# Performance work log

Hardware: AMD Instinct MI355X
Metric: run time of the kernel (lower is better)

The kernel has to match this reference:

```python
import jax, jax.numpy as jnp
import numpy as np

EPS_BN = 1e-5
EPS_W = 1e-8


def _bn(x, g, b, m, v):
    # x: [B, N, C]; params: [C] (inference-mode batchnorm)
    return g * (x - m) * jax.lax.rsqrt(v + EPS_BN) + b


def setup_inputs() -> dict:
    key = jax.random.key(0)
    ks = jax.random.split(key, 24)
    B, N, S = 16, 4096, 1024
    C1, C2 = 128, 256            # points1 / points2 channels
    CIN, COUT = C1 + C2, 128     # in_channel, out_channel

    def w(k, shape, std=0.02):
        return (jax.random.normal(k, shape, jnp.float32) * std)

    def bn_params(k, c):
        k1, k2, k3, k4 = jax.random.split(k, 4)
        return (1.0 + 0.1 * jax.random.normal(k1, (c,), jnp.float32),  # gamma
                0.1 * jax.random.normal(k2, (c,), jnp.float32),        # beta
                0.1 * jax.random.normal(k3, (c,), jnp.float32),        # running mean
                0.5 + jax.random.uniform(k4, (c,), jnp.float32))       # running var

    fg, fb, fm, fv = bn_params(ks[4], COUT)
    g1, b1, m1, v1 = bn_params(ks[5], COUT)
    g2, b2, m2, v2 = bn_params(ks[6], COUT)
    return {
        "xyz1": jax.random.uniform(ks[0], (B, N, 3), jnp.float32),
        "xyz2": jax.random.uniform(ks[1], (B, S, 3), jnp.float32),
        "points1": jax.random.normal(ks[2], (B, C1, N), jnp.float32),
        "points2": jax.random.normal(ks[3], (B, C2, S), jnp.float32),
        "fuse_w": w(ks[7], (COUT, CIN)), "fuse_b": jnp.zeros((COUT,), jnp.float32),
        "fuse_g": fg, "fuse_beta": fb, "fuse_m": fm, "fuse_v": fv,
        "c1_w": w(ks[8], (COUT, COUT)), "c1_b": jnp.zeros((COUT,), jnp.float32),
        "bn1_g": g1, "bn1_b": b1, "bn1_m": m1, "bn1_v": v1,
        "c2_w": w(ks[9], (COUT, COUT)), "c2_b": jnp.zeros((COUT,), jnp.float32),
        "bn2_g": g2, "bn2_b": b2, "bn2_m": m2, "bn2_v": v2,
    }


def reference(xyz1, xyz2, points1, points2,
              fuse_w, fuse_b, fuse_g, fuse_beta, fuse_m, fuse_v,
              c1_w, c1_b, bn1_g, bn1_b, bn1_m, bn1_v,
              c2_w, c2_b, bn2_g, bn2_b, bn2_m, bn2_v):
    B, N, _ = xyz1.shape
    pts1 = jnp.swapaxes(points1, 1, 2)   # [B, N, C1]
    pts2 = jnp.swapaxes(points2, 1, 2)   # [B, S, C2]

    # squared pairwise distances [B, N, S]
    dists = (jnp.sum(xyz1 ** 2, -1)[:, :, None]
             + jnp.sum(xyz2 ** 2, -1)[:, None, :]
             - 2.0 * jnp.einsum('bnc,bsc->bns', xyz1, xyz2))

    # 3 nearest neighbors (smallest distances)
    neg_d3, idx = jax.lax.top_k(-dists, 3)          # [B, N, 3]
    d3 = -neg_d3
    recip = 1.0 / (d3 + EPS_W)
    weight = recip / jnp.sum(recip, axis=2, keepdims=True)  # [B, N, 3]

    gathered = jax.vmap(lambda p, i: p[i])(pts2, idx)        # [B, N, 3, C2]
    interp = jnp.sum(gathered * weight[..., None], axis=2)   # [B, N, C2]

    x = jnp.concatenate([pts1, interp], axis=-1)             # [B, N, CIN]

    # fuse: 1x1 conv + BN + ReLU
    x = jax.nn.relu(_bn(jnp.einsum('bnc,oc->bno', x, fuse_w) + fuse_b,
                        fuse_g, fuse_beta, fuse_m, fuse_v))

    # residual block: conv-BN-ReLU -> conv-BN, add skip, ReLU
    h = jax.nn.relu(_bn(jnp.einsum('bnc,oc->bno', x, c1_w) + c1_b,
                        bn1_g, bn1_b, bn1_m, bn1_v))
    y = _bn(jnp.einsum('bnc,oc->bno', h, c2_w) + c2_b,
            bn2_g, bn2_b, bn2_m, bn2_v)
    out = jax.nn.relu(y + x)                                 # [B, N, COUT]
    return jnp.swapaxes(out, 1, 2)                           # [B, COUT, N]
```

## Files before the change

kernel.cpp:

```cpp
#include <hip/hip_runtime.h>
#include <hip/hip_bf16.h>

#define BB 16
#define NN 4096
#define SS 1024
#define C1 128
#define C2 256
#define CIN 384
#define CO 128

#define KCH 4
#define SCH (SS / KCH)

typedef __bf16 bf16x8 __attribute__((ext_vector_type(8)));
typedef float f32x4 __attribute__((ext_vector_type(4)));

__global__ __launch_bounds__(256) void knn_part_kernel(
    const float* __restrict__ xyz1, const float* __restrict__ xyz2,
    float4* __restrict__ pd4, int4* __restrict__ pi4)
{
    __shared__ float4 pts[SCH];
    const int b = blockIdx.z;
    const int ch = blockIdx.y;
    const float* p2 = xyz2 + ((size_t)b * SS + (size_t)ch * SCH) * 3;
    for (int i = threadIdx.x; i < SCH; i += 256) {
        float x = p2[i * 3 + 0], y = p2[i * 3 + 1], z = p2[i * 3 + 2];
        pts[i] = make_float4(x, y, z, x * x + y * y + z * z);
    }
    __syncthreads();

    const int n = blockIdx.x * 256 + threadIdx.x;
    const float* p1 = xyz1 + ((size_t)b * NN + n) * 3;
    const float x = p1[0], y = p1[1], z = p1[2];
    const float s1 = x * x + y * y + z * z;

    float d0 = 3.4e38f, d1 = 3.4e38f, d2 = 3.4e38f, d3 = 3.4e38f;
    int i0 = 0, i1 = 0, i2 = 0, i3 = 0;
    const int sbase = ch * SCH;
    #pragma unroll 4
    for (int sl = 0; sl < SCH; ++sl) {
        float4 p = pts[sl];
        float d = s1 + p.w - 2.0f * (x * p.x + y * p.y + z * p.z);
        int s = sbase + sl;
        bool lt0 = d < d0, lt1 = d < d1, lt2 = d < d2, lt3 = d < d3;
        float nd3 = lt2 ? d2 : (lt3 ? d : d3); int ni3 = lt2 ? i2 : (lt3 ? s : i3);
        float nd2 = lt1 ? d1 : (lt2 ? d : d2); int ni2 = lt1 ? i1 : (lt2 ? s : i2);
        float nd1 = lt0 ? d0 : (lt1 ? d : d1); int ni1 = lt0 ? i0 : (lt1 ? s : i1);
        d0 = lt0 ? d : d0;                     i0 = lt0 ? s : i0;
        d1 = nd1; i1 = ni1; d2 = nd2; i2 = ni2; d3 = nd3; i3 = ni3;
    }
    size_t o = ((size_t)b * NN + n) * KCH + ch;
    pd4[o] = make_float4(d0, d1, d2, d3);
    pi4[o] = make_int4(i0, i1, i2, i3);
}

__global__ __launch_bounds__(256) void knn_merge_kernel(
    const float4* __restrict__ pd4, const int4* __restrict__ pi4,
    int* __restrict__ idx4, float* __restrict__ w4)
{
    const int n = blockIdx.x * 256 + threadIdx.x;
    const int b = blockIdx.y;
    const size_t o = ((size_t)b * NN + n) * KCH;

    float d0 = 3.4e38f, d1 = 3.4e38f, d2 = 3.4e38f, d3 = 3.4e38f;
    int i0 = 0, i1 = 0, i2 = 0, i3 = 0;
    #pragma unroll
    for (int ch = 0; ch < KCH; ++ch) {
        float4 pd = pd4[o + ch];
        int4 pi = pi4[o + ch];
        float cd[4] = { pd.x, pd.y, pd.z, pd.w };
        int   ci[4] = { pi.x, pi.y, pi.z, pi.w };
        #pragma unroll
        for (int k = 0; k < 4; ++k) {
            float d = cd[k]; int s = ci[k];
            bool lt0 = d < d0, lt1 = d < d1, lt2 = d < d2, lt3 = d < d3;
            float nd3 = lt2 ? d2 : (lt3 ? d : d3); int ni3 = lt2 ? i2 : (lt3 ? s : i3);
            float nd2 = lt1 ? d1 : (lt2 ? d : d2); int ni2 = lt1 ? i1 : (lt2 ? s : i2);
            float nd1 = lt0 ? d0 : (lt1 ? d : d1); int ni1 = lt0 ? i0 : (lt1 ? s : i1);
            d0 = lt0 ? d : d0;                     i0 = lt0 ? s : i0;
            d1 = nd1; i1 = ni1; d2 = nd2; i2 = ni2; d3 = nd3; i3 = ni3;
        }
    }
    float r0 = 1.0f / (d0 + 1e-8f);
    float r1 = 1.0f / (d1 + 1e-8f);
    float r2 = 1.0f / (d2 + 1e-8f);
    float rs = r0 + r1 + r2;
    bool tie = (d2 == d3);
    size_t base = ((size_t)b * NN + n) * 4;
    idx4[base + 0] = i0; idx4[base + 1] = i1;
    idx4[base + 2] = i2; idx4[base + 3] = i3;
    w4[base + 0] = r0 / rs; w4[base + 1] = r1 / rs;
    w4[base + 2] = r2 / rs; w4[base + 3] = tie ? -1.0f : 0.0f;
}

__global__ __launch_bounds__(256) void p2t_kernel(
    const float* __restrict__ p2, float* __restrict__ p2t)
{
    __shared__ float tile[64][65];
    const int b = blockIdx.z;
    const int s0 = blockIdx.x * 64, c0 = blockIdx.y * 64;
    for (int i = threadIdx.x; i < 64 * 64; i += 256) {
        int s = i & 63, c = i >> 6;
        tile[c][s] = p2[((size_t)b * C2 + c0 + c) * SS + s0 + s];
    }
    __syncthreads();
    for (int i = threadIdx.x; i < 64 * 64; i += 256) {
        int c = i & 63, s = i >> 6;
        p2t[((size_t)b * SS + s0 + s) * C2 + c0 + c] = tile[c][s];
    }
}

__global__ __launch_bounds__(256) void wprep_kernel(
    const float* __restrict__ fw, const float* __restrict__ w1,
    const float* __restrict__ w2,
    __bf16* __restrict__ Whf, __bf16* __restrict__ Wlf,
    __bf16* __restrict__ Wh1, __bf16* __restrict__ Wl1,
    __bf16* __restrict__ Wh2, __bf16* __restrict__ Wl2)
{
    int t = blockIdx.x * 256 + threadIdx.x;
    float v; __bf16 *oh, *ol; int idx;
    if (t < 49152)      { idx = t;         v = fw[idx]; oh = Whf; ol = Wlf; }
    else if (t < 65536) { idx = t - 49152; v = w1[idx]; oh = Wh1; ol = Wl1; }
    else                { idx = t - 65536; v = w2[idx]; oh = Wh2; ol = Wl2; }
    __bf16 h = (__bf16)v;
    oh[idx] = h; ol[idx] = (__bf16)(v - (float)h);
}

__global__ __launch_bounds__(256) void tie_eval_kernel(
    const float* __restrict__ p2t, const float* __restrict__ points1,
    const int* __restrict__ idx4, float* __restrict__ w4,
    const float* __restrict__ fw, const float* __restrict__ fb,
    const float* __restrict__ fg, const float* __restrict__ fbt,
    const float* __restrict__ fm, const float* __restrict__ fv,
    const float* __restrict__ w1m, const float* __restrict__ b1,
    const float* __restrict__ g1, const float* __restrict__ bt1,
    const float* __restrict__ m1, const float* __restrict__ v1,
    const float* __restrict__ w2m, const float* __restrict__ b2,
    const float* __restrict__ g2, const float* __restrict__ bt2,
    const float* __restrict__ m2, const float* __restrict__ v2)
{
    __shared__ float Xs[4][2][CIN];
    __shared__ float XT[4][2][CO];
    __shared__ float Hs[4][2][CO];
    const int wave = threadIdx.x >> 6, lane = threadIdx.x & 63;
    const int n = blockIdx.x * 4 + wave;
    const int b = blockIdx.y;
    const size_t base = ((size_t)b * NN + n) * 4;
    if (w4[base + 3] != -1.0f) return;

    const int i0 = idx4[base + 0], i1 = idx4[base + 1];
    const int i2 = idx4[base + 2], i3 = idx4[base + 3];
    const float w0 = w4[base + 0], w1 = w4[base + 1], w2 = w4[base + 2];
    const float* P = p2t + (size_t)b * SS * C2;

    for (int c = lane; c < C1; c += 64) {
        float v = points1[((size_t)b * C1 + c) * NN + n];
        Xs[wave][0][c] = v; Xs[wave][1][c] = v;
    }
    for (int c = lane; c < C2; c += 64) {
        float f0 = P[(size_t)i0 * C2 + c], f1 = P[(size_t)i1 * C2 + c];
        float f2 = P[(size_t)i2 * C2 + c], f3 = P[(size_t)i3 * C2 + c];
        float bs = w0 * f0 + w1 * f1;
        Xs[wave][0][C1 + c] = bs + w2 * f2;
        Xs[wave][1][C1 + c] = bs + w2 * f3;
    }
    #pragma unroll
    for (int k = 0; k < 2; ++k) {
        int oc = lane + 64 * k;
        float alo = fb[oc], ahi = fb[oc];
        for (int c = 0; c < CIN; ++c) {
            float wv = fw[(size_t)oc * CIN + c];
            alo += wv * Xs[wave][0][c];
            ahi += wv * Xs[wave][1][c];
        }
        float s = fg[oc] * (1.0f / sqrtf(fv[oc] + 1e-5f));
        XT[wave][0][oc] = fmaxf(s * (alo - fm[oc]) + fbt[oc], 0.0f);
        XT[wave][1][oc] = fmaxf(s * (ahi - fm[oc]) + fbt[oc], 0.0f);
    }
    #pragma unroll
    for (int k = 0; k < 2; ++k) {
        int oc = lane + 64 * k;
        float alo = b1[oc], ahi = b1[oc];
        for (int c = 0; c < CO; ++c) {
            float wv = w1m[(size_t)oc * CO + c];
            alo += wv * XT[wave][0][c];
            ahi += wv * XT[wave][1][c];
        }
        float s = g1[oc] * (1.0f / sqrtf(v1[oc] + 1e-5f));
        Hs[wave][0][oc] = fmaxf(s * (alo - m1[oc]) + bt1[oc], 0.0f);
        Hs[wave][1][oc] = fmaxf(s * (ahi - m1[oc]) + bt1[oc], 0.0f);
    }
    float e = 0.0f;
    #pragma unroll
    for (int k = 0; k < 2; ++k) {
        int oc = lane + 64 * k;
        float alo = b2[oc], ahi = b2[oc];
        for (int c = 0; c < CO; ++c) {
            float wv = w2m[(size_t)oc * CO + c];
            alo += wv * Hs[wave][0][c];
            ahi += wv * Hs[wave][1][c];
        }
        float s = g2[oc] * (1.0f / sqrtf(v2[oc] + 1e-5f));
        float olo = fmaxf(s * (alo - m2[oc]) + bt2[oc] + XT[wave][0][oc], 0.0f);
        float ohi = fmaxf(s * (ahi - m2[oc]) + bt2[oc] + XT[wave][1][oc], 0.0f);
        e = fmaxf(e, fabsf(olo - ohi));
    }
    for (int off = 32; off; off >>= 1) e = fmaxf(e, __shfl_xor(e, off));
    if (lane == 0) {
        if (e > 0.085f) { w4[base + 3] = 0.0f; }
        else { w4[base + 2] = 0.5f * w2; w4[base + 3] = 0.5f * w2; }
    }
}

__global__ __launch_bounds__(256) void buildx_kernel(
    const float* __restrict__ points1,
    const float* __restrict__ p2t,
    const int* __restrict__ idx4, const float* __restrict__ w4,
    __bf16* __restrict__ Xh, __bf16* __restrict__ Xl)
{
    __shared__ float t1[128][66];
    const int b = blockIdx.y;
    const int n0 = blockIdx.x * 64;
    for (int i = threadIdx.x; i < 128 * 64; i += 256) {
        int j = i & 63, c = i >> 6;
        t1[c][j] = points1[((size_t)b * C1 + c) * NN + n0 + j];
    }
    __syncthreads();
    for (int i = threadIdx.x; i < 128 * 64; i += 256) {
        int c = i & 127, j = i >> 7;
        float v = t1[c][j];
        __bf16 h = (__bf16)v;
        size_t o = ((size_t)b * NN + n0 + j) * CIN + c;
        Xh[o] = h; Xl[o] = (__bf16)(v - (float)h);
    }
    for (int i = threadIdx.x; i < 64 * C2; i += 256) {
        int c = i & 255, j = i >> 8;
        int n = n0 + j;
        size_t ib = ((size_t)b * NN + n) * 4;
        int s0 = idx4[ib + 0], s1 = idx4[ib + 1];
        int s2 = idx4[ib + 2], s3 = idx4[ib + 3];
        float w0 = w4[ib + 0], w1 = w4[ib + 1];
        float w2 = w4[ib + 2], w3 = w4[ib + 3];
        const float* base = p2t + (size_t)b * SS * C2;
        float v = w0 * base[(size_t)s0 * C2 + c]
                + w1 * base[(size_t)s1 * C2 + c]
                + w2 * base[(size_t)s2 * C2 + c]
                + w3 * base[(size_t)s3 * C2 + c];
        __bf16 h = (__bf16)v;
        size_t o = ((size_t)b * NN + n) * CIN + C1 + c;
        Xh[o] = h; Xl[o] = (__bf16)(v - (float)h);
    }
}

template<int K, int MODE>
__global__ __launch_bounds__(256) void gemm_bn_kernel(
    const __bf16* __restrict__ Ah, const __bf16* __restrict__ Al,
    const __bf16* __restrict__ Wh, const __bf16* __restrict__ Wl,
    const float* __restrict__ cb,  const float* __restrict__ gg,
    const float* __restrict__ bbta, const float* __restrict__ mm,
    const float* __restrict__ vv,
    const __bf16* __restrict__ skiph, const __bf16* __restrict__ skipl,
    __bf16* __restrict__ outh, __bf16* __restrict__ outl,
    float* __restrict__ outf)
{
    __shared__ __attribute__((aligned(16))) __bf16 wls_h[128 * 40];
    __shared__ __attribute__((aligned(16))) __bf16 wls_l[128 * 40];
    __shared__ float s_s[128], s_t[128];
    __shared__ float tile[32][132];
    const int tid = threadIdx.x;
    if (tid < 128) {
        float s = gg[tid] * (1.0f / sqrtf(vv[tid] + 1e-5f));
        float t = (cb[tid] - mm[tid]) * s + bbta[tid];
        s_s[tid] = s; s_t[tid] = t;
    }
    const int wave = tid >> 6, lane = tid & 63;
    const int m = lane & 15, q = lane >> 4;
    const size_t r0 = (size_t)blockIdx.x * 128 + wave * 32;

    f32x4 acc[2][8] = {};
    const __bf16* pAh = Ah + (r0 + m) * (size_t)K + q * 8;
    const __bf16* pAl = Al + (r0 + m) * (size_t)K + q * 8;

    const int wrow = tid >> 1, whf = tid & 1;
    for (int kk = 0; kk < K; kk += 32) {
        __syncthreads();
        {
            size_t g = (size_t)wrow * K + kk + whf * 16;
            int lo = wrow * 40 + whf * 16;
            *(uint4*)&wls_h[lo]     = *(const uint4*)&Wh[g];
            *(uint4*)&wls_h[lo + 8] = *(const uint4*)&Wh[g + 8];
            *(uint4*)&wls_l[lo]     = *(const uint4*)&Wl[g];
            *(uint4*)&wls_l[lo + 8] = *(const uint4*)&Wl[g + 8];
        }
        __syncthreads();
        bf16x8 ah0 = *(const bf16x8*)(pAh + kk);
        bf16x8 al0 = *(const bf16x8*)(pAl + kk);
        bf16x8 ah1 = *(const bf16x8*)(pAh + 16 * (size_t)K + kk);
        bf16x8 al1 = *(const bf16x8*)(pAl + 16 * (size_t)K + kk);
        #pragma unroll
        for (int ot = 0; ot < 8; ++ot) {
            bf16x8 bh = *(const bf16x8*)&wls_h[(ot * 16 + m) * 40 + q * 8];
            bf16x8 bl = *(const bf16x8*)&wls_l[(ot * 16 + m) * 40 + q * 8];
            acc[0][ot] = __builtin_amdgcn_mfma_f32_16x16x32_bf16(ah0, bh, acc[0][ot], 0, 0, 0);
            acc[0][ot] = __builtin_amdgcn_mfma_f32_16x16x32_bf16(al0, bh, acc[0][ot], 0, 0, 0);
            acc[0][ot] = __builtin_amdgcn_mfma_f32_16x16x32_bf16(ah0, bl, acc[0][ot], 0, 0, 0);
            acc[1][ot] = __builtin_amdgcn_mfma_f32_16x16x32_bf16(ah1, bh, acc[1][ot], 0, 0, 0);
            acc[1][ot] = __builtin_amdgcn_mfma_f32_16x16x32_bf16(al1, bh, acc[1][ot], 0, 0, 0);
            acc[1][ot] = __builtin_amdgcn_mfma_f32_16x16x32_bf16(ah1, bl, acc[1][ot], 0, 0, 0);
        }
    }

    if (MODE == 0) {
        #pragma unroll
        for (int rt = 0; rt < 2; ++rt) {
            #pragma unroll
            for (int ot = 0; ot < 8; ++ot) {
                int col = ot * 16 + m;
                float sc = s_s[col], sh = s_t[col];
                #pragma unroll
                for (int r = 0; r < 4; ++r) {
                    size_t row = r0 + rt * 16 + q * 4 + r;
                    float val = fmaxf(acc[rt][ot][r] * sc + sh, 0.0f);
                    __bf16 h = (__bf16)val;
                    outh[row * 128 + col] = h;
                    outl[row * 128 + col] = (__bf16)(val - (float)h);
                }
            }
        }
    } else {
        const int bidx = (int)(((size_t)blockIdx.x * 128) >> 12);
        const int nbase = (int)(((size_t)blockIdx.x * 128) & 4095);
        for (int cc = 0; cc < 4; ++cc) {
            __syncthreads();
            #pragma unroll
            for (int oo = 0; oo < 2; ++oo) {
                int ot = cc * 2 + oo;
                int col = ot * 16 + m;
                float sc = s_s[col], sh = s_t[col];
                #pragma unroll
                for (int rt = 0; rt < 2; ++rt) {
                    #pragma unroll
                    for (int r = 0; r < 4; ++r) {
                        int lrow = wave * 32 + rt * 16 + q * 4 + r;
                        size_t row = (size_t)blockIdx.x * 128 + lrow;
                        float val = acc[rt][ot][r] * sc + sh;
                        val += (float)skiph[row * 128 + col] + (float)skipl[row * 128 + col];
                        val = fmaxf(val, 0.0f);
                        tile[oo * 16 + m][lrow] = val;
                    }
                }
            }
            __syncthreads();
            for (int c2 = tid >> 7; c2 < 32; c2 += 2) {
                int nn_ = tid & 127;
                outf[((size_t)bidx * 128 + cc * 32 + c2) * NN + nbase + nn_] = tile[c2][nn_];
            }
        }
    }
}

extern "C" void kernel_launch(void* const* d_in, const int* in_sizes, int n_in,
                              void* d_out, int out_size, void* d_ws, size_t ws_size,
                              hipStream_t stream) {
    const float* xyz1    = (const float*)d_in[0];
    const float* xyz2    = (const float*)d_in[1];
    const float* points1 = (const float*)d_in[2];
    const float* points2 = (const float*)d_in[3];
    const float* fuse_w  = (const float*)d_in[4];
    const float* fuse_b  = (const float*)d_in[5];
    const float* fuse_g  = (const float*)d_in[6];
    const float* fuse_bt = (const float*)d_in[7];
    const float* fuse_m  = (const float*)d_in[8];
    const float* fuse_v  = (const float*)d_in[9];
    const float* c1_w    = (const float*)d_in[10];
    const float* c1_b    = (const float*)d_in[11];
    const float* bn1_g   = (const float*)d_in[12];
    const float* bn1_b   = (const float*)d_in[13];
    const float* bn1_m   = (const float*)d_in[14];
    const float* bn1_v   = (const float*)d_in[15];
    const float* c2_w    = (const float*)d_in[16];
    const float* c2_b    = (const float*)d_in[17];
    const float* bn2_g   = (const float*)d_in[18];
    const float* bn2_b   = (const float*)d_in[19];
    const float* bn2_m   = (const float*)d_in[20];
    const float* bn2_v   = (const float*)d_in[21];

    char* ws = (char*)d_ws;
    int*    idx4 = (int*)(ws);
    float*  w4   = (float*)(ws + 1048576);
    float*  p2t  = (float*)(ws + 2097152);
    __bf16* Xh   = (__bf16*)(ws + 18874368);
    __bf16* Xl   = (__bf16*)(ws + 69206016);
    __bf16* Y0h  = (__bf16*)(ws + 119537664);
    __bf16* Y0l  = (__bf16*)(ws + 136314880);
    __bf16* Hh   = (__bf16*)(ws + 153092096);
    __bf16* Hl   = (__bf16*)(ws + 169869312);
    __bf16* Whf  = (__bf16*)(ws + 186646528);
    __bf16* Wlf  = (__bf16*)(ws + 186744832);
    __bf16* Wh1  = (__bf16*)(ws + 186843136);
    __bf16* Wl1  = (__bf16*)(ws + 186875904);
    __bf16* Wh2  = (__bf16*)(ws + 186908672);
    __bf16* Wl2  = (__bf16*)(ws + 186941440);

    float4* pd4 = (float4*)(ws + 18874368);
    int4*   pi4 = (int4*)(ws + 18874368 + 4194304);

    knn_part_kernel<<<dim3(NN / 256, KCH, BB), 256, 0, stream>>>(xyz1, xyz2, pd4, pi4);
    knn_merge_kernel<<<dim3(NN / 256, BB), 256, 0, stream>>>(pd4, pi4, idx4, w4);
    p2t_kernel<<<dim3(SS / 64, C2 / 64, BB), 256, 0, stream>>>(points2, p2t);
    wprep_kernel<<<320, 256, 0, stream>>>(fuse_w, c1_w, c2_w,
                                          Whf, Wlf, Wh1, Wl1, Wh2, Wl2);
    tie_eval_kernel<<<dim3(NN / 4, BB), 256, 0, stream>>>(
        p2t, points1, idx4, w4,
        fuse_w, fuse_b, fuse_g, fuse_bt, fuse_m, fuse_v,
        c1_w, c1_b, bn1_g, bn1_b, bn1_m, bn1_v,
        c2_w, c2_b, bn2_g, bn2_b, bn2_m, bn2_v);
    buildx_kernel<<<dim3(NN / 64, BB), 256, 0, stream>>>(points1, p2t, idx4, w4, Xh, Xl);

    const int gblocks = (BB * NN) / 128;
    gemm_bn_kernel<CIN, 0><<<gblocks, 256, 0, stream>>>(
        Xh, Xl, Whf, Wlf, fuse_b, fuse_g, fuse_bt, fuse_m, fuse_v,
        nullptr, nullptr, Y0h, Y0l, nullptr);
    gemm_bn_kernel<CO, 0><<<gblocks, 256, 0, stream>>>(
        Y0h, Y0l, Wh1, Wl1, c1_b, bn1_g, bn1_b, bn1_m, bn1_v,
        nullptr, nullptr, Hh, Hl, nullptr);
    gemm_bn_kernel<CO, 1><<<gblocks, 256, 0, stream>>>(
        Hh, Hl, Wh2, Wl2, c2_b, bn2_g, bn2_b, bn2_m, bn2_v,
        Y0h, Y0l, nullptr, nullptr, (float*)d_out);
}
```

Before: 354.8 us.

## Fuse interpolation and concat into first GEMM, doubling KNN chunk split

Removes the buildx kernel and its bf16 hi/lo X buffers. A new fused GEMM kernel reads points1 directly and computes the weighted 3-NN interpolation from p2t per K-slice, splitting into bf16 hi/lo in registers before the MFMAs. This avoids writing and re-reading the large concatenated input. The KNN partial kernel also splits the reference set into 8 chunks instead of 4, adding parallelism at the cost of more merge work. The gathers are now inside the GEMM loop without prefetching, which may expose latency.

```diff
diff --git a/kernel.cpp b/kernel.cpp
--- a/kernel.cpp
+++ b/kernel.cpp
@@ -9,7 +9,7 @@
 #define CIN 384
 #define CO 128
 
-#define KCH 4
+#define KCH 8
 #define SCH (SS / KCH)
 
 typedef __bf16 bf16x8 __attribute__((ext_vector_type(8)));
@@ -212,43 +212,141 @@
     }
 }
 
-__global__ __launch_bounds__(256) void buildx_kernel(
-    const float* __restrict__ points1,
-    const float* __restrict__ p2t,
+__global__ __launch_bounds__(256) void gemm1f_kernel(
+    const float* __restrict__ points1, const float* __restrict__ p2t,
     const int* __restrict__ idx4, const float* __restrict__ w4,
-    __bf16* __restrict__ Xh, __bf16* __restrict__ Xl)
-{
-    __shared__ float t1[128][66];
-    const int b = blockIdx.y;
-    const int n0 = blockIdx.x * 64;
-    for (int i = threadIdx.x; i < 128 * 64; i += 256) {
-        int j = i & 63, c = i >> 6;
-        t1[c][j] = points1[((size_t)b * C1 + c) * NN + n0 + j];
-    }
-    __syncthreads();
-    for (int i = threadIdx.x; i < 128 * 64; i += 256) {
-        int c = i & 127, j = i >> 7;
-        float v = t1[c][j];
-        __bf16 h = (__bf16)v;
-        size_t o = ((size_t)b * NN + n0 + j) * CIN + c;
-        Xh[o] = h; Xl[o] = (__bf16)(v - (float)h);
-    }
-    for (int i = threadIdx.x; i < 64 * C2; i += 256) {
-        int c = i & 255, j = i >> 8;
-        int n = n0 + j;
-        size_t ib = ((size_t)b * NN + n) * 4;
-        int s0 = idx4[ib + 0], s1 = idx4[ib + 1];
-        int s2 = idx4[ib + 2], s3 = idx4[ib + 3];
-        float w0 = w4[ib + 0], w1 = w4[ib + 1];
-        float w2 = w4[ib + 2], w3 = w4[ib + 3];
-        const float* base = p2t + (size_t)b * SS * C2;
-        float v = w0 * base[(size_t)s0 * C2 + c]
-                + w1 * base[(size_t)s1 * C2 + c]
-                + w2 * base[(size_t)s2 * C2 + c]
-                + w3 * base[(size_t)s3 * C2 + c];
-        __bf16 h = (__bf16)v;
-        size_t o = ((size_t)b * NN + n) * CIN + C1 + c;
-        Xh[o] = h; Xl[o] = (__bf16)(v - (float)h);
+    const __bf16* __restrict__ Wh, const __bf16* __restrict__ Wl,
+    const float* __restrict__ cb,  const float* __restrict__ gg,
+    const float* __restrict__ bbta, const float* __restrict__ mm,
+    const float* __restrict__ vv,
+    __bf16* __restrict__ outh, __bf16* __restrict__ outl)
+{
+    __shared__ __attribute__((aligned(16))) __bf16 wls_h[128 * 40];
+    __shared__ __attribute__((aligned(16))) __bf16 wls_l[128 * 40];
+    __shared__ float s_s[128], s_t[128];
+    const int tid = threadIdx.x;
+    if (tid < 128) {
+        float s = gg[tid] * (1.0f / sqrtf(vv[tid] + 1e-5f));
+        float t = (cb[tid] - mm[tid]) * s + bbta[tid];
+        s_s[tid] = s; s_t[tid] = t;
+    }
+    const int bid = (blockIdx.x & 7) * 64 + (blockIdx.x >> 3);
+    const int b = bid >> 5;
+    const int nbase = (bid & 31) * 128;
+    const int wave = tid >> 6, lane = tid & 63;
+    const int m = lane & 15, q = lane >> 4;
+
+    const size_t pa = (size_t)b * NN + nbase + wave * 32 + m;
+    const int4   ia4 = *(const int4*)&idx4[pa * 4];
+    const float4 wa4 = *(const float4*)&w4[pa * 4];
+    const int4   ib4 = *(const int4*)&idx4[(pa + 16) * 4];
+    const float4 wb4 = *(const float4*)&w4[(pa + 16) * 4];
+    const float* P = p2t + (size_t)b * SS * C2;
+
+    f32x4 acc[2][8] = {};
+    const int wrow = tid >> 1, whf = tid & 1;
+
+    for (int kk = 0; kk < CIN; kk += 32) {
+        __syncthreads();
+        {
+            size_t g = (size_t)wrow * CIN + kk + whf * 16;
+            int lo = wrow * 40 + whf * 16;
+            *(uint4*)&wls_h[lo]     = *(const uint4*)&Wh[g];
+            *(uint4*)&wls_h[lo + 8] = *(const uint4*)&Wh[g + 8];
+            *(uint4*)&wls_l[lo]     = *(const uint4*)&Wl[g];
+            *(uint4*)&wls_l[lo + 8] = *(const uint4*)&Wl[g + 8];
+        }
+        __syncthreads();
+
+        bf16x8 ah0, al0, ah1, al1;
+        if (kk < C1) {
+            const float* p1 = points1 + ((size_t)b * C1 + kk + q * 8) * NN
+                            + nbase + wave * 32 + m;
+            #pragma unroll
+            for (int j = 0; j < 8; ++j) {
+                float v = p1[(size_t)j * NN];
+                __bf16 h = (__bf16)v;
+                ah0[j] = h; al0[j] = (__bf16)(v - (float)h);
+            }
+            #pragma unroll
+            for (int j = 0; j < 8; ++j) {
+                float v = p1[(size_t)j * NN + 16];
+                __bf16 h = (__bf16)v;
+                ah1[j] = h; al1[j] = (__bf16)(v - (float)h);
+            }
+        } else {
+            const int c0 = kk - C1 + q * 8;
+            const float* g0 = P + (size_t)ia4.x * C2 + c0;
+            const float* g1 = P + (size_t)ia4.y * C2 + c0;
+            const float* g2 = P + (size_t)ia4.z * C2 + c0;
+            const float* g3 = P + (size_t)ia4.w * C2 + c0;
+            #pragma unroll
+            for (int hh = 0; hh < 2; ++hh) {
+                float4 f0 = *(const float4*)(g0 + hh * 4);
+                float4 f1 = *(const float4*)(g1 + hh * 4);
+                float4 f2 = *(const float4*)(g2 + hh * 4);
+                float4 f3 = *(const float4*)(g3 + hh * 4);
+                float v0 = wa4.x * f0.x + wa4.y * f1.x + wa4.z * f2.x + wa4.w * f3.x;
+                float v1 = wa4.x * f0.y + wa4.y * f1.y + wa4.z * f2.y + wa4.w * f3.y;
+                float v2 = wa4.x * f0.z + wa4.y * f1.z + wa4.z * f2.z + wa4.w * f3.z;
+                float v3 = wa4.x * f0.w + wa4.y * f1.w + wa4.z * f2.w + wa4.w * f3.w;
+                __bf16 h0 = (__bf16)v0, h1 = (__bf16)v1, h2 = (__bf16)v2, h3 = (__bf16)v3;
+                ah0[hh * 4 + 0] = h0; al0[hh * 4 + 0] = (__bf16)(v0 - (float)h0);
+                ah0[hh * 4 + 1] = h1; al0[hh * 4 + 1] = (__bf16)(v1 - (float)h1);
+                ah0[hh * 4 + 2] = h2; al0[hh * 4 + 2] = (__bf16)(v2 - (float)h2);
+                ah0[hh * 4 + 3] = h3; al0[hh * 4 + 3] = (__bf16)(v3 - (float)h3);
+            }
+            const float* e0 = P + (size_t)ib4.x * C2 + c0;
+            const float* e1 = P + (size_t)ib4.y * C2 + c0;
+            const float* e2 = P + (size_t)ib4.z * C2 + c0;
+            const float* e3 = P + (size_t)ib4.w * C2 + c0;
+            #pragma unroll
+            for (int hh = 0; hh < 2; ++hh) {
+                float4 f0 = *(const float4*)(e0 + hh * 4);
+                float4 f1 = *(const float4*)(e1 + hh * 4);
+                float4 f2 = *(const float4*)(e2 + hh * 4);
+                float4 f3 = *(const float4*)(e3 + hh * 4);
+                float v0 = wb4.x * f0.x + wb4.y * f1.x + wb4.z * f2.x + wb4.w * f3.x;
+                float v1 = wb4.x * f0.y + wb4.y * f1.y + wb4.z * f2.y + wb4.w * f3.y;
+                float v2 = wb4.x * f0.z + wb4.y * f1.z + wb4.z * f2.z + wb4.w * f3.z;
+                float v3 = wb4.x * f0.w + wb4.y * f1.w + wb4.z * f2.w + wb4.w * f3.w;
+                __bf16 h0 = (__bf16)v0, h1 = (__bf16)v1, h2 = (__bf16)v2, h3 = (__bf16)v3;
+                ah1[hh * 4 + 0] = h0; al1[hh * 4 + 0] = (__bf16)(v0 - (float)h0);
+                ah1[hh * 4 + 1] = h1; al1[hh * 4 + 1] = (__bf16)(v1 - (float)h1);
+                ah1[hh * 4 + 2] = h2; al1[hh * 4 + 2] = (__bf16)(v2 - (float)h2);
+                ah1[hh * 4 + 3] = h3; al1[hh * 4 + 3] = (__bf16)(v3 - (float)h3);
+            }
+        }
+
+        #pragma unroll
+        for (int ot = 0; ot < 8; ++ot) {
+            bf16x8 bh = *(const bf16x8*)&wls_h[(ot * 16 + m) * 40 + q * 8];
+            bf16x8 bl = *(const bf16x8*)&wls_l[(ot * 16 + m) * 40 + q * 8];
+            acc[0][ot] = __builtin_amdgcn_mfma_f32_16x16x32_bf16(ah0, bh, acc[0][ot], 0, 0, 0);
+            acc[0][ot] = __builtin_amdgcn_mfma_f32_16x16x32_bf16(al0, bh, acc[0][ot], 0, 0, 0);
+            acc[0][ot] = __builtin_amdgcn_mfma_f32_16x16x32_bf16(ah0, bl, acc[0][ot], 0, 0, 0);
+            acc[1][ot] = __builtin_amdgcn_mfma_f32_16x16x32_bf16(ah1, bh, acc[1][ot], 0, 0, 0);
+            acc[1][ot] = __builtin_amdgcn_mfma_f32_16x16x32_bf16(al1, bh, acc[1][ot], 0, 0, 0);
+            acc[1][ot] = __builtin_amdgcn_mfma_f32_16x16x32_bf16(ah1, bl, acc[1][ot], 0, 0, 0);
+        }
+    }
+
+    const size_t r0 = (size_t)bid * 128 + wave * 32;
+    #pragma unroll
+    for (int rt = 0; rt < 2; ++rt) {
+        #pragma unroll
+        for (int ot = 0; ot < 8; ++ot) {
+            int col = ot * 16 + m;
+            float sc = s_s[col], sh = s_t[col];
+            #pragma unroll
+            for (int r = 0; r < 4; ++r) {
+                size_t row = r0 + rt * 16 + q * 4 + r;
+                float val = fmaxf(acc[rt][ot][r] * sc + sh, 0.0f);
+                __bf16 h = (__bf16)val;
+                outh[row * 128 + col] = h;
+                outl[row * 128 + col] = (__bf16)(val - (float)h);
+            }
+        }
     }
 }
 
@@ -389,8 +487,6 @@
     int*    idx4 = (int*)(ws);
     float*  w4   = (float*)(ws + 1048576);
     float*  p2t  = (float*)(ws + 2097152);
-    __bf16* Xh   = (__bf16*)(ws + 18874368);
-    __bf16* Xl   = (__bf16*)(ws + 69206016);
     __bf16* Y0h  = (__bf16*)(ws + 119537664);
     __bf16* Y0l  = (__bf16*)(ws + 136314880);
     __bf16* Hh   = (__bf16*)(ws + 153092096);
@@ -403,7 +499,7 @@
     __bf16* Wl2  = (__bf16*)(ws + 186941440);
 
     float4* pd4 = (float4*)(ws + 18874368);
-    int4*   pi4 = (int4*)(ws + 18874368 + 4194304);
+    int4*   pi4 = (int4*)(ws + 18874368 + 8388608);
 
     knn_part_kernel<<<dim3(NN / 256, KCH, BB), 256, 0, stream>>>(xyz1, xyz2, pd4, pi4);
     knn_merge_kernel<<<dim3(NN / 256, BB), 256, 0, stream>>>(pd4, pi4, idx4, w4);
@@ -415,12 +511,11 @@
         fuse_w, fuse_b, fuse_g, fuse_bt, fuse_m, fuse_v,
         c1_w, c1_b, bn1_g, bn1_b, bn1_m, bn1_v,
         c2_w, c2_b, bn2_g, bn2_b, bn2_m, bn2_v);
-    buildx_kernel<<<dim3(NN / 64, BB), 256, 0, stream>>>(points1, p2t, idx4, w4, Xh, Xl);
 
     const int gblocks = (BB * NN) / 128;
-    gemm_bn_kernel<CIN, 0><<<gblocks, 256, 0, stream>>>(
-        Xh, Xl, Whf, Wlf, fuse_b, fuse_g, fuse_bt, fuse_m, fuse_v,
-        nullptr, nullptr, Y0h, Y0l, nullptr);
+    gemm1f_kernel<<<gblocks, 256, 0, stream>>>(
+        points1, p2t, idx4, w4, Whf, Wlf,
+        fuse_b, fuse_g, fuse_bt, fuse_m, fuse_v, Y0h, Y0l);
     gemm_bn_kernel<CO, 0><<<gblocks, 256, 0, stream>>>(
         Y0h, Y0l, Wh1, Wl1, c1_b, bn1_g, bn1_b, bn1_m, bn1_v,
         nullptr, nullptr, Hh, Hl, nullptr);
```

New measurement: 315.1 us. -11.2%, faster.
